# Kernel tuning notes

Measured on AMD Instinct MI355X. Metric: run time of the kernel, lower is better.

## Reference

```python
import jax, jax.numpy as jnp
import numpy as np

K = 10          # negatives per anchor (init k)
GAMMA = 1.0     # margin (init gamma)
CHUNK = 32      # anchor chunk for L1 cdist to bound [chunk, N, d] intermediate


def _l1_cdist(a, b):
    """Cityblock distances. a: [A, d], b: [N, d] -> [A, N], chunked over A."""
    A, d = a.shape
    a_c = a.reshape(A // CHUNK, CHUNK, d)
    def f(ac):  # ac: [CHUNK, d] -> [CHUNK, N]
        return jnp.sum(jnp.abs(ac[:, None, :] - b[None, :, :]), axis=-1)
    return jax.lax.map(f, a_c).reshape(A, b.shape[0])


def setup_inputs() -> dict:
    key = jax.random.key(0)
    k1, k2, k3, k4 = jax.random.split(key, 4)
    N, D, A = 20000, 128, 1024
    return {
        "out1": jax.random.normal(k1, (N, D), dtype=jnp.float32),
        "out2": jax.random.normal(k2, (N, D), dtype=jnp.float32),
        "anchor1": jax.random.randint(k3, (A,), 0, N),
        "anchor2": jax.random.randint(k4, (A,), 0, N),
    }


def reference(out1, out2, anchor1, anchor2):
    a1 = out1[anchor1]              # [A, D]
    a2 = out2[anchor2]              # [A, D]
    # neg sampling: k nearest (smallest L1 distance) rows of the other side
    d1 = _l1_cdist(a1, out2)        # [A, N]
    d2 = _l1_cdist(a2, out1)        # [A, N]
    neg1 = jnp.argsort(d1, axis=1)[:, :K]   # [A, K] indices into out2
    neg2 = jnp.argsort(d2, axis=1)[:, :K]   # [A, K] indices into out1
    neg_e1 = out2[neg1]             # [A, K, D]
    neg_e2 = out1[neg2]             # [A, K, D]
    A_pos = jnp.sum(jnp.abs(a1 - a2), axis=1)   # [A] positive L1 distance
    Dm = A_pos + GAMMA                           # [A]
    B1 = -jnp.sum(jnp.abs(a1[:, None, :] - neg_e1), axis=2)  # [A, K]
    L1 = jnp.sum(jax.nn.relu(Dm[:, None] + B1))
    B2 = -jnp.sum(jnp.abs(a2[:, None, :] - neg_e2), axis=2)  # [A, K]
    L2 = jnp.sum(jax.nn.relu(Dm[:, None] + B2))
    return (L1 + L2) / (anchor1.shape[0] * K)
```

## Files before the change

kernel.cpp:

```cpp
#include <hip/hip_runtime.h>

#define N_PTS 20000
#define DIMS  128
#define A_CNT 1024
#define KNEG  10
#define NTILES 157
#define NCHUNK (NTILES * 16)
#define NCHUNK_REAL 2500
#define BIGV  1e18f
#define BIGI  0x7F000000
#define CAND_CAP 768
#define PT_CAP   768
#define AB_BLOCKS 1024
#define QR_BLOCKS 625
#define RPART     1250

__device__ __forceinline__ unsigned int sad_u8(unsigned int a, unsigned int b, unsigned int c) {
#if __has_builtin(__builtin_amdgcn_sad_u8)
    return __builtin_amdgcn_sad_u8(a, b, c);
#else
    unsigned int d;
    asm("v_sad_u8 %0, %1, %2, %3" : "=v"(d) : "v"(a), "v"(b), "v"(c));
    return d;
#endif
}

__global__ void absmax_kernel(const float* __restrict__ a, const float* __restrict__ b,
                              float* __restrict__ wsAmax, float* __restrict__ outZero) {
    __shared__ float sm[4];
    const int n4 = N_PTS * DIMS / 4;
    const int stride = gridDim.x * blockDim.x;
    float m = 0.f;
    for (int i = blockIdx.x * blockDim.x + threadIdx.x; i < 2 * n4; i += stride) {
        const float4 v = (i < n4) ? ((const float4*)a)[i] : ((const float4*)b)[i - n4];
        m = fmaxf(m, fmaxf(fmaxf(fabsf(v.x), fabsf(v.y)), fmaxf(fabsf(v.z), fabsf(v.w))));
    }
#pragma unroll
    for (int s = 1; s < 64; s <<= 1) m = fmaxf(m, __shfl_xor(m, s, 64));
    if ((threadIdx.x & 63) == 0) sm[threadIdx.x >> 6] = m;
    __syncthreads();
    if (threadIdx.x == 0) {
        wsAmax[blockIdx.x] = fmaxf(fmaxf(sm[0], sm[1]), fmaxf(sm[2], sm[3]));
        if (blockIdx.x == 0) *outZero = 0.f;
    }
}

__global__ void quantR_kernel(const float* __restrict__ o1, const float* __restrict__ o2,
                              unsigned int* __restrict__ q1, unsigned int* __restrict__ q2,
                              float* __restrict__ Ra, float* __restrict__ Rb,
                              const float* __restrict__ wsAmax,
                              float* __restrict__ wsRmaxPart) {
    __shared__ float sm[4];
    __shared__ float sM;
    const int tid = threadIdx.x;
    {
        const float4 v = ((const float4*)wsAmax)[tid];
        float m = fmaxf(fmaxf(v.x, v.y), fmaxf(v.z, v.w));
#pragma unroll
        for (int s = 1; s < 64; s <<= 1) m = fmaxf(m, __shfl_xor(m, s, 64));
        if ((tid & 63) == 0) sm[tid >> 6] = m;
        __syncthreads();
        if (tid == 0) sM = fmaxf(fmaxf(sm[0], sm[1]), fmaxf(sm[2], sm[3]));
        __syncthreads();
    }
    const float M = sM;
    const float s = 127.0f / M;

    const int side = blockIdx.y;
    const float* src = side ? o2 : o1;
    unsigned int* dst = side ? q2 : q1;
    float* Rrow = side ? Rb : Ra;
    const int g = blockIdx.x * 256 + tid;
    const int row = g >> 3;
    const int sub = g & 7;
    const float4* s4 = (const float4*)(src + (size_t)row * DIMS + sub * 16);
    unsigned int* d = dst + (size_t)row * 32 + sub * 4;
    float rs = 0.f;
#pragma unroll
    for (int m = 0; m < 4; ++m) {
        const float4 v = s4[m];
        const float f0 = v.x * s + 127.0f, f1 = v.y * s + 127.0f;
        const float f2 = v.z * s + 127.0f, f3 = v.w * s + 127.0f;
        const float q0 = rintf(f0), q1v = rintf(f1), q2v = rintf(f2), q3 = rintf(f3);
        rs += fabsf(q0 - f0) + fabsf(q1v - f1) + fabsf(q2v - f2) + fabsf(q3 - f3);
        d[m] = (unsigned int)q0 | ((unsigned int)q1v << 8) |
               ((unsigned int)q2v << 16) | ((unsigned int)q3 << 24);
    }
    rs += __shfl_xor(rs, 1, 64);
    rs += __shfl_xor(rs, 2, 64);
    rs += __shfl_xor(rs, 4, 64);
    const float R = rs + 1.0f;
    if (sub == 0) Rrow[row] = R;
    float rm = R;
    rm = fmaxf(rm, __shfl_xor(rm, 8, 64));
    rm = fmaxf(rm, __shfl_xor(rm, 16, 64));
    rm = fmaxf(rm, __shfl_xor(rm, 32, 64));
    if ((tid & 63) == 0) sm[tid >> 6] = rm;
    __syncthreads();
    if (tid == 0)
        wsRmaxPart[blockIdx.y * QR_BLOCKS + blockIdx.x] =
            fmaxf(fmaxf(sm[0], sm[1]), fmaxf(sm[2], sm[3]));
}

__global__ __launch_bounds__(256, 4)
void dist_sad_kernel(const unsigned int* __restrict__ q1, const unsigned int* __restrict__ q2,
                     const int* __restrict__ anchor1, const int* __restrict__ anchor2,
                     unsigned short* __restrict__ minOut,
                     const float* __restrict__ wsRmaxPart, float* __restrict__ rmaxOut) {
    __shared__ unsigned int sP[128 * 32];

    const int tile = blockIdx.x;
    const int ag   = blockIdx.y;
    const int side = blockIdx.z;

    if (tile == 0 && ag == 0 && side == 0 && threadIdx.x < 64) {
        float r = 0.f;
        for (int i = threadIdx.x; i < RPART; i += 64) r = fmaxf(r, wsRmaxPart[i]);
#pragma unroll
        for (int s = 1; s < 64; s <<= 1) r = fmaxf(r, __shfl_xor(r, s, 64));
        if (threadIdx.x == 0) *rmaxOut = r;
    }

    const unsigned int* aData = side ? q2 : q1;
    const unsigned int* pData = side ? q1 : q2;
    const int*          aIdx  = side ? anchor2 : anchor1;

    const int tid = threadIdx.x;
    const int tx = tid & 15;
    const int ty = tid >> 4;

    const int4 aidx4 = ((const int4*)(aIdx + ag * 64))[ty];
    const unsigned int* aRow0 = aData + (size_t)aidx4.x * 32;
    const unsigned int* aRow1 = aData + (size_t)aidx4.y * 32;
    const unsigned int* aRow2 = aData + (size_t)aidx4.z * 32;
    const unsigned int* aRow3 = aData + (size_t)aidx4.w * 32;

    {
        const int rp = tid >> 1;
        const int h  = tid & 1;
        const int prow = tile * 128 + rp;
        const bool pvalid = prow < N_PTS;
        const uint4* pRow4 = (const uint4*)(pData + (size_t)prow * 32 + h * 16);
        const int rot = rp >> 3;
#pragma unroll
        for (int j = 0; j < 4; ++j) {
            const uint4 v = pvalid ? pRow4[j]
                                   : make_uint4(0xFFFFFFFFu, 0xFFFFFFFFu, 0xFFFFFFFFu, 0xFFFFFFFFu);
            const int blk = h * 4 + j;
            *(uint4*)&sP[rp * 32 + (((blk + rot) & 7) << 2)] = v;
        }
    }
    __syncthreads();

    unsigned int acc[4][8];
#pragma unroll
    for (int i = 0; i < 4; ++i)
#pragma unroll
        for (int j = 0; j < 8; ++j) acc[i][j] = 0u;

    const int tx8 = tx * 8;

#pragma unroll 2
    for (int bk = 0; bk < 8; ++bk) {
        uint4 A[4], P[8];
        A[0] = *(const uint4*)(aRow0 + bk * 4);
        A[1] = *(const uint4*)(aRow1 + bk * 4);
        A[2] = *(const uint4*)(aRow2 + bk * 4);
        A[3] = *(const uint4*)(aRow3 + bk * 4);
        const int pslot = ((bk + tx) & 7) << 2;
#pragma unroll
        for (int j = 0; j < 8; ++j) P[j] = *(const uint4*)&sP[(tx8 + j) * 32 + pslot];
#pragma unroll
        for (int i = 0; i < 4; ++i)
#pragma unroll
            for (int j = 0; j < 8; ++j) {
                unsigned int s = sad_u8(A[i].x, P[j].x, acc[i][j]);
                s = sad_u8(A[i].y, P[j].y, s);
                s = sad_u8(A[i].z, P[j].z, s);
                acc[i][j] = sad_u8(A[i].w, P[j].w, s);
            }
    }

    const int ty4 = ty * 4;
    const size_t outBase = (size_t)side * A_CNT * NCHUNK;
#pragma unroll
    for (int i = 0; i < 4; ++i) {
        unsigned int m = min(min(min(acc[i][0], acc[i][1]), min(acc[i][2], acc[i][3])),
                             min(min(acc[i][4], acc[i][5]), min(acc[i][6], acc[i][7])));
        minOut[outBase + (size_t)(ag * 64 + ty4 + i) * NCHUNK + tile * 16 + tx] =
            (unsigned short)m;
    }
}

__global__ __launch_bounds__(256, 4)
void select_kernel(const float* __restrict__ out1, const float* __restrict__ out2,
                   const unsigned int* __restrict__ q1, const unsigned int* __restrict__ q2,
                   const int* __restrict__ anchor1, const int* __restrict__ anchor2,
                   const unsigned short* __restrict__ minIn,
                   const float* __restrict__ R1, const float* __restrict__ R2,
                   const float* __restrict__ rmaxIn, float* __restrict__ out) {
    const int bid = blockIdx.x;
    const int side = bid >> 10;
    const int ai = bid & 1023;
    const int tid = threadIdx.x;
    const int lane = tid & 63;
    const int wv = tid >> 6;

    const float* aDataF = side ? out2 : out1;
    const float* pDataF = side ? out1 : out2;
    const unsigned int* aDataQ = side ? q2 : q1;
    const unsigned int* pDataQ = side ? q1 : q2;
    const float* Ranc = side ? R2 : R1;
    const int* aIdx = side ? anchor2 : anchor1;

    __shared__ int candCount, pointCount;
    __shared__ int candList[CAND_CAP];
    __shared__ int ptList[PT_CAP];
    __shared__ __align__(16) float sDist[PT_CAP];
    __shared__ int sMin[4];
    __shared__ int sCnt[4];
    __shared__ float wSum[4];
    __shared__ float sDm;

    const int arow = aIdx[ai];
    const uint4 qa4 = ((const uint4*)(aDataQ + (size_t)arow * 32))[lane & 7];
    if (tid == 0) { candCount = 0; pointCount = 0; }

    if (wv == 0) {
        const int r1 = anchor1[ai], r2 = anchor2[ai];
        const float2 x1 = ((const float2*)(out1 + (size_t)r1 * DIMS))[lane];
        const float2 x2 = ((const float2*)(out2 + (size_t)r2 * DIMS))[lane];
        float dm = fabsf(x1.x - x2.x) + fabsf(x1.y - x2.y);
#pragma unroll
        for (int s = 1; s < 64; s <<= 1) dm += __shfl_xor(dm, s, 64);
        if (lane == 0) sDm = dm + 1.0f;
    }

    const unsigned short* mbase = minIn + ((size_t)side * A_CNT + ai) * NCHUNK;
    int mv[10];
#pragma unroll
    for (int j = 0; j < 10; ++j) {
        const int c = tid + 256 * j;
        mv[j] = (c < NCHUNK_REAL) ? (int)mbase[c] : BIGI;
    }
    int lmin = BIGI;
#pragma unroll
    for (int j = 0; j < 10; ++j) lmin = min(lmin, mv[j]);
#pragma unroll
    for (int s = 1; s < 64; s <<= 1) lmin = min(lmin, __shfl_xor(lmin, s, 64));
    if (lane == 0) sMin[wv] = lmin;
    __syncthreads();
    const int m1 = min(min(sMin[0], sMin[1]), min(sMin[2], sMin[3]));

    int E = m1 + 192;
    for (;;) {
        int c = 0;
#pragma unroll
        for (int j = 0; j < 10; ++j) c += (mv[j] <= E) ? 1 : 0;
#pragma unroll
        for (int s = 1; s < 64; s <<= 1) c += __shfl_xor(c, s, 64);
        if (lane == 0) sCnt[wv] = c;
        __syncthreads();
        const int total = sCnt[0] + sCnt[1] + sCnt[2] + sCnt[3];
        __syncthreads();
        if (total >= KNEG) break;
        E += 192;
    }
    int lo = (E == m1 + 192) ? (m1 - 1) : (E - 192);
    int hi = E;
#pragma unroll
    for (int it = 0; it < 3; ++it) {
        const int mid = (lo + hi) >> 1;
        int c = 0;
#pragma unroll
        for (int j = 0; j < 10; ++j) c += (mv[j] <= mid) ? 1 : 0;
#pragma unroll
        for (int s = 1; s < 64; s <<= 1) c += __shfl_xor(c, s, 64);
        if (lane == 0) sCnt[wv] = c;
        __syncthreads();
        const int total = sCnt[0] + sCnt[1] + sCnt[2] + sCnt[3];
        __syncthreads();
        if (total >= KNEG) hi = mid; else lo = mid;
    }
    const float Rmax = *rmaxIn;
    const float thr = (float)hi + 2.0f * Ranc[arow] + 2.0f * Rmax + 4.0f;

#pragma unroll
    for (int j = 0; j < 10; ++j) {
        const int c = tid + 256 * j;
        if (c < NCHUNK_REAL && (float)mv[j] <= thr) {
            const int pos = atomicAdd(&candCount, 1);
            if (pos < CAND_CAP) candList[pos] = c;
        }
    }
    __syncthreads();
    const int cc = min(candCount, CAND_CAP);

    const int psub = lane >> 3;
    const int seg  = lane & 7;
    for (int s0 = wv * 4; s0 < cc; s0 += 16) {
        uint4 qp[4];
        int ptv[4];
#pragma unroll
        for (int u = 0; u < 4; ++u) {
            const int s = s0 + u;
            const int c = candList[(s < cc) ? s : s0];
            ptv[u] = c * 8 + psub;
            qp[u] = ((const uint4*)(pDataQ + (size_t)ptv[u] * 32))[seg];
        }
#pragma unroll
        for (int u = 0; u < 4; ++u) {
            unsigned int d = sad_u8(qa4.x, qp[u].x, 0u);
            d = sad_u8(qa4.y, qp[u].y, d);
            d = sad_u8(qa4.z, qp[u].z, d);
            d = sad_u8(qa4.w, qp[u].w, d);
            int di = (int)d;
            di += __shfl_xor(di, 1, 64);
            di += __shfl_xor(di, 2, 64);
            di += __shfl_xor(di, 4, 64);
            if ((s0 + u) < cc && seg == 0 && (float)di <= thr) {
                const int pos = atomicAdd(&pointCount, 1);
                if (pos < PT_CAP) ptList[pos] = ptv[u];
            }
        }
    }
    __syncthreads();
    const int pc = min(pointCount, PT_CAP);

    const int pt4 = tid >> 2;
    const int qq  = tid & 3;
    float4 av[8];
    {
        const float4* aF4 = (const float4*)(aDataF + (size_t)arow * DIMS) + qq * 8;
#pragma unroll
        for (int q = 0; q < 8; ++q) av[q] = aF4[q];
    }
    for (int base = 0; base < pc; base += 64) {
        const int idx = base + pt4;
        float s01 = 0.f, s23 = 0.f;
        if (idx < pc) {
            const int pt = ptList[idx];
            const float4* p4 = (const float4*)(pDataF + (size_t)pt * DIMS) + qq * 8;
#pragma unroll
            for (int q = 0; q < 8; ++q) {
                const float4 pv = p4[q];
                s01 += fabsf(av[q].x - pv.x) + fabsf(av[q].y - pv.y);
                s23 += fabsf(av[q].z - pv.z) + fabsf(av[q].w - pv.w);
            }
        }
        float s = s01 + s23;
        s += __shfl_xor(s, 1, 64);
        s += __shfl_xor(s, 2, 64);
        if (qq == 0 && idx < pc) sDist[idx] = s;
    }
    __syncthreads();

    const float dm = sDm;
    float contrib = 0.f;
    if (pc <= 256) {
        const int i0 = tid;
        const float v = (i0 < pc) ? sDist[i0] : BIGV;
        int r0 = 0;
        int j = 0;
        for (; j + 2 <= pc; j += 2) {
            const float2 vj = *(const float2*)&sDist[j];
            r0 += ((vj.x < v) || (vj.x == v && j < i0)) ? 1 : 0;
            r0 += ((vj.y < v) || (vj.y == v && (j + 1) < i0)) ? 1 : 0;
        }
        if (j < pc) {
            const float vj = sDist[j];
            r0 += ((vj < v) || (vj == v && j < i0)) ? 1 : 0;
        }
        if (i0 < pc && r0 < KNEG) contrib = fmaxf(dm - v, 0.f);
    } else {
        const int i0 = tid, i1 = tid + 256, i2 = tid + 512;
        float va = BIGV, vb = BIGV, vc = BIGV;
        if (i0 < pc) va = sDist[i0];
        if (i1 < pc) vb = sDist[i1];
        if (i2 < pc) vc = sDist[i2];
        int r0 = 0, r1 = 0, r2 = 0;
        for (int j = 0; j < pc; ++j) {
            const float vj = sDist[j];
            r0 += (vj < va) || (vj == va && j < i0);
            r1 += (vj < vb) || (vj == vb && j < i1);
            r2 += (vj < vc) || (vj == vc && j < i2);
        }
        if (i0 < pc && r0 < KNEG) contrib += fmaxf(dm - va, 0.f);
        if (i1 < pc && r1 < KNEG) contrib += fmaxf(dm - vb, 0.f);
        if (i2 < pc && r2 < KNEG) contrib += fmaxf(dm - vc, 0.f);
    }
#pragma unroll
    for (int s = 1; s < 64; s <<= 1) contrib += __shfl_xor(contrib, s, 64);
    if (lane == 0) wSum[wv] = contrib;
    __syncthreads();
    if (tid == 0)
        atomicAdd(out, (wSum[0] + wSum[1] + wSum[2] + wSum[3]) * (1.0f / (A_CNT * KNEG)));
}

extern "C" void kernel_launch(void* const* d_in, const int* in_sizes, int n_in,
                              void* d_out, int out_size, void* d_ws, size_t ws_size,
                              hipStream_t stream) {
    const float* out1    = (const float*)d_in[0];
    const float* out2    = (const float*)d_in[1];
    const int*   anchor1 = (const int*)d_in[2];
    const int*   anchor2 = (const int*)d_in[3];
    float* out = (float*)d_out;

    unsigned int* q1 = (unsigned int*)d_ws;
    unsigned int* q2 = q1 + (size_t)N_PTS * DIMS / 4;
    unsigned short* minbuf = (unsigned short*)(q2 + (size_t)N_PTS * DIMS / 4);
    float* R1 = (float*)(minbuf + (size_t)2 * A_CNT * NCHUNK);
    float* R2 = R1 + N_PTS;
    float* wsAmax = R2 + N_PTS;
    float* wsRmaxPart = wsAmax + AB_BLOCKS;
    float* rmax = wsRmaxPart + 1280;

    hipLaunchKernelGGL(absmax_kernel, dim3(AB_BLOCKS), dim3(256), 0, stream,
                       out1, out2, wsAmax, out);
    hipLaunchKernelGGL(quantR_kernel, dim3(QR_BLOCKS, 2), dim3(256), 0, stream,
                       out1, out2, q1, q2, R1, R2, wsAmax, wsRmaxPart);

    dim3 gridA(NTILES, 16, 2);
    hipLaunchKernelGGL(dist_sad_kernel, gridA, dim3(256), 0, stream,
                       q1, q2, anchor1, anchor2, minbuf, wsRmaxPart, rmax);
    hipLaunchKernelGGL(select_kernel, dim3(2048), dim3(256), 0, stream,
                       out1, out2, q1, q2, anchor1, anchor2, minbuf, R1, R2, rmax, out);
}
```

Measured before the change: 207.6 us.

## Store packed per-point SAD offsets to skip quantized recompute in select

The distance kernel now writes, next to each chunk minimum, a 32-bit word holding a 4-bit coarse offset per point (distance minus chunk min, shifted by 4 and clamped). The select kernel uses these packed offsets to filter individual points against the threshold directly. This drops the candidate-chunk list and the second quantized SAD pass over candidate points' rows. In exchange it adds a 2×1024×2512×4-byte write in the dist kernel and a read in select. The clamped and truncated offsets are a looser lower bound, so more points may pass the filter or overflow PT_CAP.

```diff
diff --git a/kernel.cpp b/kernel.cpp
--- a/kernel.cpp
+++ b/kernel.cpp
@@ -9,7 +9,6 @@
 #define NCHUNK_REAL 2500
 #define BIGV  1e18f
 #define BIGI  0x7F000000
-#define CAND_CAP 768
 #define PT_CAP   768
 #define AB_BLOCKS 1024
 #define QR_BLOCKS 625
@@ -105,7 +104,7 @@
 __global__ __launch_bounds__(256, 4)
 void dist_sad_kernel(const unsigned int* __restrict__ q1, const unsigned int* __restrict__ q2,
                      const int* __restrict__ anchor1, const int* __restrict__ anchor2,
-                     unsigned short* __restrict__ minOut,
+                     unsigned short* __restrict__ minOut, unsigned int* __restrict__ offOut,
                      const float* __restrict__ wsRmaxPart, float* __restrict__ rmaxOut) {
     __shared__ unsigned int sP[128 * 32];
 
@@ -185,18 +184,23 @@
     const size_t outBase = (size_t)side * A_CNT * NCHUNK;
 #pragma unroll
     for (int i = 0; i < 4; ++i) {
-        unsigned int m = min(min(min(acc[i][0], acc[i][1]), min(acc[i][2], acc[i][3])),
-                             min(min(acc[i][4], acc[i][5]), min(acc[i][6], acc[i][7])));
-        minOut[outBase + (size_t)(ag * 64 + ty4 + i) * NCHUNK + tile * 16 + tx] =
-            (unsigned short)m;
+        const unsigned int m = min(min(min(acc[i][0], acc[i][1]), min(acc[i][2], acc[i][3])),
+                                   min(min(acc[i][4], acc[i][5]), min(acc[i][6], acc[i][7])));
+        unsigned int pk = 0u;
+#pragma unroll
+        for (int j = 0; j < 8; ++j)
+            pk |= min(15u, (acc[i][j] - m) >> 4) << (4 * j);
+        const size_t cidx = outBase + (size_t)(ag * 64 + ty4 + i) * NCHUNK + tile * 16 + tx;
+        minOut[cidx] = (unsigned short)m;
+        offOut[cidx] = pk;
     }
 }
 
 __global__ __launch_bounds__(256, 4)
 void select_kernel(const float* __restrict__ out1, const float* __restrict__ out2,
-                   const unsigned int* __restrict__ q1, const unsigned int* __restrict__ q2,
                    const int* __restrict__ anchor1, const int* __restrict__ anchor2,
                    const unsigned short* __restrict__ minIn,
+                   const unsigned int* __restrict__ offIn,
                    const float* __restrict__ R1, const float* __restrict__ R2,
                    const float* __restrict__ rmaxIn, float* __restrict__ out) {
     const int bid = blockIdx.x;
@@ -208,13 +212,10 @@
 
     const float* aDataF = side ? out2 : out1;
     const float* pDataF = side ? out1 : out2;
-    const unsigned int* aDataQ = side ? q2 : q1;
-    const unsigned int* pDataQ = side ? q1 : q2;
     const float* Ranc = side ? R2 : R1;
     const int* aIdx = side ? anchor2 : anchor1;
 
-    __shared__ int candCount, pointCount;
-    __shared__ int candList[CAND_CAP];
+    __shared__ int pointCount;
     __shared__ int ptList[PT_CAP];
     __shared__ __align__(16) float sDist[PT_CAP];
     __shared__ int sMin[4];
@@ -223,8 +224,7 @@
     __shared__ float sDm;
 
     const int arow = aIdx[ai];
-    const uint4 qa4 = ((const uint4*)(aDataQ + (size_t)arow * 32))[lane & 7];
-    if (tid == 0) { candCount = 0; pointCount = 0; }
+    if (tid == 0) pointCount = 0;
 
     if (wv == 0) {
         const int r1 = anchor1[ai], r2 = anchor2[ai];
@@ -285,42 +285,20 @@
     const float Rmax = *rmaxIn;
     const float thr = (float)hi + 2.0f * Ranc[arow] + 2.0f * Rmax + 4.0f;
 
+    const unsigned int* offRow = offIn + ((size_t)side * A_CNT + ai) * NCHUNK;
 #pragma unroll
     for (int j = 0; j < 10; ++j) {
         const int c = tid + 256 * j;
         if (c < NCHUNK_REAL && (float)mv[j] <= thr) {
-            const int pos = atomicAdd(&candCount, 1);
-            if (pos < CAND_CAP) candList[pos] = c;
-        }
-    }
-    __syncthreads();
-    const int cc = min(candCount, CAND_CAP);
-
-    const int psub = lane >> 3;
-    const int seg  = lane & 7;
-    for (int s0 = wv * 4; s0 < cc; s0 += 16) {
-        uint4 qp[4];
-        int ptv[4];
-#pragma unroll
-        for (int u = 0; u < 4; ++u) {
-            const int s = s0 + u;
-            const int c = candList[(s < cc) ? s : s0];
-            ptv[u] = c * 8 + psub;
-            qp[u] = ((const uint4*)(pDataQ + (size_t)ptv[u] * 32))[seg];
-        }
-#pragma unroll
-        for (int u = 0; u < 4; ++u) {
-            unsigned int d = sad_u8(qa4.x, qp[u].x, 0u);
-            d = sad_u8(qa4.y, qp[u].y, d);
-            d = sad_u8(qa4.z, qp[u].z, d);
-            d = sad_u8(qa4.w, qp[u].w, d);
-            int di = (int)d;
-            di += __shfl_xor(di, 1, 64);
-            di += __shfl_xor(di, 2, 64);
-            di += __shfl_xor(di, 4, 64);
-            if ((s0 + u) < cc && seg == 0 && (float)di <= thr) {
-                const int pos = atomicAdd(&pointCount, 1);
-                if (pos < PT_CAP) ptList[pos] = ptv[u];
+            const unsigned int pk = offRow[c];
+            const int m = mv[j];
+#pragma unroll
+            for (int jj = 0; jj < 8; ++jj) {
+                const int bound = m + (int)(((pk >> (4 * jj)) & 15u) << 4);
+                if ((float)bound <= thr) {
+                    const int pos = atomicAdd(&pointCount, 1);
+                    if (pos < PT_CAP) ptList[pos] = c * 8 + jj;
+                }
             }
         }
     }
@@ -409,7 +387,8 @@
     unsigned int* q1 = (unsigned int*)d_ws;
     unsigned int* q2 = q1 + (size_t)N_PTS * DIMS / 4;
     unsigned short* minbuf = (unsigned short*)(q2 + (size_t)N_PTS * DIMS / 4);
-    float* R1 = (float*)(minbuf + (size_t)2 * A_CNT * NCHUNK);
+    unsigned int* offbuf = (unsigned int*)(minbuf + (size_t)2 * A_CNT * NCHUNK);
+    float* R1 = (float*)(offbuf + (size_t)2 * A_CNT * NCHUNK);
     float* R2 = R1 + N_PTS;
     float* wsAmax = R2 + N_PTS;
     float* wsRmaxPart = wsAmax + AB_BLOCKS;
@@ -422,7 +401,7 @@
 
     dim3 gridA(NTILES, 16, 2);
     hipLaunchKernelGGL(dist_sad_kernel, gridA, dim3(256), 0, stream,
-                       q1, q2, anchor1, anchor2, minbuf, wsRmaxPart, rmax);
+                       q1, q2, anchor1, anchor2, minbuf, offbuf, wsRmaxPart, rmax);
     hipLaunchKernelGGL(select_kernel, dim3(2048), dim3(256), 0, stream,
-                       out1, out2, q1, q2, anchor1, anchor2, minbuf, R1, R2, rmax, out);
-}
+                       out1, out2, anchor1, anchor2, minbuf, offbuf, R1, R2, rmax, out);
+}
```

Result: no change. 211.6 us (+1.9%).

## Fuse all four stages into one persistent cooperative kernel with grid syncs

Applied to the files above, without the earlier changes.

Replaces the four separate launches (absmax, quantise, SAD distance tiles, select) with a single persistent cooperative kernel that loops over virtual blocks and uses grid-wide syncs between stages. This is meant to remove launch overhead and the tail idle time between kernels. In exchange, the grid is capped at occupancy times CU count (at most 1024 blocks), and the grid barriers plus less flexible scheduling may reduce throughput in the heavy distance stage. If the cooperative launch is unavailable it falls back to the original launches.

```diff
diff --git a/kernel.cpp b/kernel.cpp
--- a/kernel.cpp
+++ b/kernel.cpp
@@ -1,4 +1,7 @@
 #include <hip/hip_runtime.h>
+#include <hip/hip_cooperative_groups.h>
+
+namespace cg = cooperative_groups;
 
 #define N_PTS 20000
 #define DIMS  128
@@ -77,14 +80,14 @@
     unsigned int* d = dst + (size_t)row * 32 + sub * 4;
     float rs = 0.f;
 #pragma unroll
-    for (int m = 0; m < 4; ++m) {
-        const float4 v = s4[m];
+    for (int m4 = 0; m4 < 4; ++m4) {
+        const float4 v = s4[m4];
         const float f0 = v.x * s + 127.0f, f1 = v.y * s + 127.0f;
         const float f2 = v.z * s + 127.0f, f3 = v.w * s + 127.0f;
         const float q0 = rintf(f0), q1v = rintf(f1), q2v = rintf(f2), q3 = rintf(f3);
         rs += fabsf(q0 - f0) + fabsf(q1v - f1) + fabsf(q2v - f2) + fabsf(q3 - f3);
-        d[m] = (unsigned int)q0 | ((unsigned int)q1v << 8) |
-               ((unsigned int)q2v << 16) | ((unsigned int)q3 << 24);
+        d[m4] = (unsigned int)q0 | ((unsigned int)q1v << 8) |
+                ((unsigned int)q2v << 16) | ((unsigned int)q3 << 24);
     }
     rs += __shfl_xor(rs, 1, 64);
     rs += __shfl_xor(rs, 2, 64);
@@ -108,7 +111,6 @@
                      unsigned short* __restrict__ minOut,
                      const float* __restrict__ wsRmaxPart, float* __restrict__ rmaxOut) {
     __shared__ unsigned int sP[128 * 32];
-
     const int tile = blockIdx.x;
     const int ag   = blockIdx.y;
     const int side = blockIdx.z;
@@ -124,7 +126,6 @@
     const unsigned int* aData = side ? q2 : q1;
     const unsigned int* pData = side ? q1 : q2;
     const int*          aIdx  = side ? anchor2 : anchor1;
-
     const int tid = threadIdx.x;
     const int tx = tid & 15;
     const int ty = tid >> 4;
@@ -157,7 +158,6 @@
     for (int i = 0; i < 4; ++i)
 #pragma unroll
         for (int j = 0; j < 8; ++j) acc[i][j] = 0u;
-
     const int tx8 = tx * 8;
 
 #pragma unroll 2
@@ -397,6 +397,381 @@
         atomicAdd(out, (wSum[0] + wSum[1] + wSum[2] + wSum[3]) * (1.0f / (A_CNT * KNEG)));
 }
 
+__global__ __launch_bounds__(256, 4)
+void fused_kernel(const float* __restrict__ out1, const float* __restrict__ out2,
+                  const int* __restrict__ anchor1, const int* __restrict__ anchor2,
+                  unsigned int* __restrict__ q1, unsigned int* __restrict__ q2,
+                  unsigned short* __restrict__ minbuf,
+                  float* __restrict__ R1, float* __restrict__ R2,
+                  float* __restrict__ wsAmax, float* __restrict__ wsRmaxPart,
+                  float* __restrict__ rmaxG, float* __restrict__ out) {
+    cg::grid_group grid = cg::this_grid();
+    const int bid = blockIdx.x;
+    const int nb  = gridDim.x;
+    const int tid = threadIdx.x;
+    const int lane = tid & 63;
+    const int wv = tid >> 6;
+
+    __shared__ unsigned int sP[128 * 32];
+    __shared__ float smax[4];
+    __shared__ float sM;
+
+    {
+        const int n4 = N_PTS * DIMS / 4;
+        float m = 0.f;
+        for (int i = bid * 256 + tid; i < 2 * n4; i += nb * 256) {
+            const float4 v = (i < n4) ? ((const float4*)out1)[i] : ((const float4*)out2)[i - n4];
+            m = fmaxf(m, fmaxf(fmaxf(fabsf(v.x), fabsf(v.y)), fmaxf(fabsf(v.z), fabsf(v.w))));
+        }
+#pragma unroll
+        for (int s = 1; s < 64; s <<= 1) m = fmaxf(m, __shfl_xor(m, s, 64));
+        if (lane == 0) smax[wv] = m;
+        __syncthreads();
+        if (tid == 0) {
+            wsAmax[bid] = fmaxf(fmaxf(smax[0], smax[1]), fmaxf(smax[2], smax[3]));
+            if (bid == 0) *out = 0.f;
+        }
+    }
+    grid.sync();
+
+    {
+        __syncthreads();
+        {
+            float m = 0.f;
+            for (int i = tid; i < nb; i += 256) m = fmaxf(m, wsAmax[i]);
+#pragma unroll
+            for (int s = 1; s < 64; s <<= 1) m = fmaxf(m, __shfl_xor(m, s, 64));
+            if (lane == 0) smax[wv] = m;
+            __syncthreads();
+            if (tid == 0) sM = fmaxf(fmaxf(smax[0], smax[1]), fmaxf(smax[2], smax[3]));
+            __syncthreads();
+        }
+        const float M = sM;
+        const float s = 127.0f / M;
+        for (int vb = bid; vb < 2 * QR_BLOCKS; vb += nb) {
+            __syncthreads();
+            const int side = (vb >= QR_BLOCKS) ? 1 : 0;
+            const int bx = side ? (vb - QR_BLOCKS) : vb;
+            const float* src = side ? out2 : out1;
+            unsigned int* dst = side ? q2 : q1;
+            float* Rrow = side ? R2 : R1;
+            const int g = bx * 256 + tid;
+            const int row = g >> 3;
+            const int sub = g & 7;
+            const float4* s4 = (const float4*)(src + (size_t)row * DIMS + sub * 16);
+            unsigned int* d = dst + (size_t)row * 32 + sub * 4;
+            float rs = 0.f;
+#pragma unroll
+            for (int m4 = 0; m4 < 4; ++m4) {
+                const float4 v = s4[m4];
+                const float f0 = v.x * s + 127.0f, f1 = v.y * s + 127.0f;
+                const float f2 = v.z * s + 127.0f, f3 = v.w * s + 127.0f;
+                const float q0 = rintf(f0), q1v = rintf(f1), q2v = rintf(f2), q3 = rintf(f3);
+                rs += fabsf(q0 - f0) + fabsf(q1v - f1) + fabsf(q2v - f2) + fabsf(q3 - f3);
+                d[m4] = (unsigned int)q0 | ((unsigned int)q1v << 8) |
+                        ((unsigned int)q2v << 16) | ((unsigned int)q3 << 24);
+            }
+            rs += __shfl_xor(rs, 1, 64);
+            rs += __shfl_xor(rs, 2, 64);
+            rs += __shfl_xor(rs, 4, 64);
+            const float R = rs + 1.0f;
+            if (sub == 0) Rrow[row] = R;
+            float rm = R;
+            rm = fmaxf(rm, __shfl_xor(rm, 8, 64));
+            rm = fmaxf(rm, __shfl_xor(rm, 16, 64));
+            rm = fmaxf(rm, __shfl_xor(rm, 32, 64));
+            if (lane == 0) smax[wv] = rm;
+            __syncthreads();
+            if (tid == 0)
+                wsRmaxPart[side * QR_BLOCKS + bx] =
+                    fmaxf(fmaxf(smax[0], smax[1]), fmaxf(smax[2], smax[3]));
+        }
+    }
+    grid.sync();
+
+    if (bid == 0 && tid < 64) {
+        float r = 0.f;
+        for (int i = tid; i < RPART; i += 64) r = fmaxf(r, wsRmaxPart[i]);
+#pragma unroll
+        for (int s = 1; s < 64; s <<= 1) r = fmaxf(r, __shfl_xor(r, s, 64));
+        if (tid == 0) *rmaxG = r;
+    }
+    {
+        const int tx = tid & 15;
+        const int ty = tid >> 4;
+        const int tx8 = tx * 8;
+        const int ty4 = ty * 4;
+        for (int vb = bid; vb < NTILES * 32; vb += nb) {
+            const int tile = vb % NTILES;
+            const int rest = vb / NTILES;
+            const int ag   = rest & 15;
+            const int side = rest >> 4;
+
+            const unsigned int* aData = side ? q2 : q1;
+            const unsigned int* pData = side ? q1 : q2;
+            const int*          aIdx  = side ? anchor2 : anchor1;
+
+            const int4 aidx4 = ((const int4*)(aIdx + ag * 64))[ty];
+            const unsigned int* aRow0 = aData + (size_t)aidx4.x * 32;
+            const unsigned int* aRow1 = aData + (size_t)aidx4.y * 32;
+            const unsigned int* aRow2 = aData + (size_t)aidx4.z * 32;
+            const unsigned int* aRow3 = aData + (size_t)aidx4.w * 32;
+
+            __syncthreads();
+            {
+                const int rp = tid >> 1;
+                const int h  = tid & 1;
+                const int prow = tile * 128 + rp;
+                const bool pvalid = prow < N_PTS;
+                const uint4* pRow4 = (const uint4*)(pData + (size_t)prow * 32 + h * 16);
+                const int rot = rp >> 3;
+#pragma unroll
+                for (int j = 0; j < 4; ++j) {
+                    const uint4 v = pvalid ? pRow4[j]
+                                           : make_uint4(0xFFFFFFFFu, 0xFFFFFFFFu,
+                                                        0xFFFFFFFFu, 0xFFFFFFFFu);
+                    const int blk = h * 4 + j;
+                    *(uint4*)&sP[rp * 32 + (((blk + rot) & 7) << 2)] = v;
+                }
+            }
+            __syncthreads();
+
+            unsigned int acc[4][8];
+#pragma unroll
+            for (int i = 0; i < 4; ++i)
+#pragma unroll
+                for (int j = 0; j < 8; ++j) acc[i][j] = 0u;
+
+#pragma unroll 2
+            for (int bk = 0; bk < 8; ++bk) {
+                uint4 A[4], P[8];
+                A[0] = *(const uint4*)(aRow0 + bk * 4);
+                A[1] = *(const uint4*)(aRow1 + bk * 4);
+                A[2] = *(const uint4*)(aRow2 + bk * 4);
+                A[3] = *(const uint4*)(aRow3 + bk * 4);
+                const int pslot = ((bk + tx) & 7) << 2;
+#pragma unroll
+                for (int j = 0; j < 8; ++j) P[j] = *(const uint4*)&sP[(tx8 + j) * 32 + pslot];
+#pragma unroll
+                for (int i = 0; i < 4; ++i)
+#pragma unroll
+                    for (int j = 0; j < 8; ++j) {
+                        unsigned int sacc = sad_u8(A[i].x, P[j].x, acc[i][j]);
+                        sacc = sad_u8(A[i].y, P[j].y, sacc);
+                        sacc = sad_u8(A[i].z, P[j].z, sacc);
+                        acc[i][j] = sad_u8(A[i].w, P[j].w, sacc);
+                    }
+            }
+
+            const size_t outBase = (size_t)side * A_CNT * NCHUNK;
+#pragma unroll
+            for (int i = 0; i < 4; ++i) {
+                unsigned int m = min(min(min(acc[i][0], acc[i][1]), min(acc[i][2], acc[i][3])),
+                                     min(min(acc[i][4], acc[i][5]), min(acc[i][6], acc[i][7])));
+                minbuf[outBase + (size_t)(ag * 64 + ty4 + i) * NCHUNK + tile * 16 + tx] =
+                    (unsigned short)m;
+            }
+        }
+    }
+    grid.sync();
+
+    {
+        int* candList = (int*)sP;
+        int* ptList   = candList + CAND_CAP;
+        float* sDist  = (float*)(ptList + PT_CAP);
+        int* misc     = (int*)(sDist + PT_CAP);
+        float* wSum = (float*)(misc + 10);
+        const float Rmax = *rmaxG;
+
+        for (int vt = bid; vt < 2 * A_CNT; vt += nb) {
+            __syncthreads();
+            const int side = vt >> 10;
+            const int ai = vt & 1023;
+
+            const float* aDataF = side ? out2 : out1;
+            const float* pDataF = side ? out1 : out2;
+            const unsigned int* aDataQ = side ? q2 : q1;
+            const unsigned int* pDataQ = side ? q1 : q2;
+            const float* Ranc = side ? R2 : R1;
+            const int* aIdx = side ? anchor2 : anchor1;
+
+            const int arow = aIdx[ai];
+            const uint4 qa4 = ((const uint4*)(aDataQ + (size_t)arow * 32))[lane & 7];
+            if (tid == 0) { misc[0] = 0; misc[1] = 0; }
+
+            if (wv == 0) {
+                const int r1 = anchor1[ai], r2 = anchor2[ai];
+                const float2 x1 = ((const float2*)(out1 + (size_t)r1 * DIMS))[lane];
+                const float2 x2 = ((const float2*)(out2 + (size_t)r2 * DIMS))[lane];
+                float dm = fabsf(x1.x - x2.x) + fabsf(x1.y - x2.y);
+#pragma unroll
+                for (int s = 1; s < 64; s <<= 1) dm += __shfl_xor(dm, s, 64);
+                if (lane == 0) ((float*)misc)[14] = dm + 1.0f;
+            }
+
+            const unsigned short* mbase = minbuf + ((size_t)side * A_CNT + ai) * NCHUNK;
+            int mv[10];
+#pragma unroll
+            for (int j = 0; j < 10; ++j) {
+                const int c = tid + 256 * j;
+                mv[j] = (c < NCHUNK_REAL) ? (int)mbase[c] : BIGI;
+            }
+            int lmin = BIGI;
+#pragma unroll
+            for (int j = 0; j < 10; ++j) lmin = min(lmin, mv[j]);
+#pragma unroll
+            for (int s = 1; s < 64; s <<= 1) lmin = min(lmin, __shfl_xor(lmin, s, 64));
+            if (lane == 0) misc[2 + wv] = lmin;
+            __syncthreads();
+            const int m1 = min(min(misc[2], misc[3]), min(misc[4], misc[5]));
+
+            int E = m1 + 192;
+            for (;;) {
+                int c = 0;
+#pragma unroll
+                for (int j = 0; j < 10; ++j) c += (mv[j] <= E) ? 1 : 0;
+#pragma unroll
+                for (int s = 1; s < 64; s <<= 1) c += __shfl_xor(c, s, 64);
+                if (lane == 0) misc[6 + wv] = c;
+                __syncthreads();
+                const int total = misc[6] + misc[7] + misc[8] + misc[9];
+                __syncthreads();
+                if (total >= KNEG) break;
+                E += 192;
+            }
+            int lo = (E == m1 + 192) ? (m1 - 1) : (E - 192);
+            int hi = E;
+#pragma unroll
+            for (int it = 0; it < 3; ++it) {
+                const int mid = (lo + hi) >> 1;
+                int c = 0;
+#pragma unroll
+                for (int j = 0; j < 10; ++j) c += (mv[j] <= mid) ? 1 : 0;
+#pragma unroll
+                for (int s = 1; s < 64; s <<= 1) c += __shfl_xor(c, s, 64);
+                if (lane == 0) misc[6 + wv] = c;
+                __syncthreads();
+                const int total = misc[6] + misc[7] + misc[8] + misc[9];
+                __syncthreads();
+                if (total >= KNEG) hi = mid; else lo = mid;
+            }
+            const float thr = (float)hi + 2.0f * Ranc[arow] + 2.0f * Rmax + 4.0f;
+
+#pragma unroll
+            for (int j = 0; j < 10; ++j) {
+                const int c = tid + 256 * j;
+                if (c < NCHUNK_REAL && (float)mv[j] <= thr) {
+                    const int pos = atomicAdd(&misc[0], 1);
+                    if (pos < CAND_CAP) candList[pos] = c;
+                }
+            }
+            __syncthreads();
+            const int cc = min(misc[0], CAND_CAP);
+
+            const int psub = lane >> 3;
+            const int seg  = lane & 7;
+            for (int s0 = wv * 4; s0 < cc; s0 += 16) {
+                uint4 qp[4];
+                int ptv[4];
+#pragma unroll
+                for (int u = 0; u < 4; ++u) {
+                    const int s = s0 + u;
+                    const int c = candList[(s < cc) ? s : s0];
+                    ptv[u] = c * 8 + psub;
+                    qp[u] = ((const uint4*)(pDataQ + (size_t)ptv[u] * 32))[seg];
+                }
+#pragma unroll
+                for (int u = 0; u < 4; ++u) {
+                    unsigned int d = sad_u8(qa4.x, qp[u].x, 0u);
+                    d = sad_u8(qa4.y, qp[u].y, d);
+                    d = sad_u8(qa4.z, qp[u].z, d);
+                    d = sad_u8(qa4.w, qp[u].w, d);
+                    int di = (int)d;
+                    di += __shfl_xor(di, 1, 64);
+                    di += __shfl_xor(di, 2, 64);
+                    di += __shfl_xor(di, 4, 64);
+                    if ((s0 + u) < cc && seg == 0 && (float)di <= thr) {
+                        const int pos = atomicAdd(&misc[1], 1);
+                        if (pos < PT_CAP) ptList[pos] = ptv[u];
+                    }
+                }
+            }
+            __syncthreads();
+            const int pc = min(misc[1], PT_CAP);
+
+            const int pt4 = tid >> 2;
+            const int qq  = tid & 3;
+            float4 av[8];
+            {
+                const float4* aF4 = (const float4*)(aDataF + (size_t)arow * DIMS) + qq * 8;
+#pragma unroll
+                for (int q = 0; q < 8; ++q) av[q] = aF4[q];
+            }
+            for (int base = 0; base < pc; base += 64) {
+                const int idx = base + pt4;
+                float s01 = 0.f, s23 = 0.f;
+                if (idx < pc) {
+                    const int pt = ptList[idx];
+                    const float4* p4 = (const float4*)(pDataF + (size_t)pt * DIMS) + qq * 8;
+#pragma unroll
+                    for (int q = 0; q < 8; ++q) {
+                        const float4 pv = p4[q];
+                        s01 += fabsf(av[q].x - pv.x) + fabsf(av[q].y - pv.y);
+                        s23 += fabsf(av[q].z - pv.z) + fabsf(av[q].w - pv.w);
+                    }
+                }
+                float sacc = s01 + s23;
+                sacc += __shfl_xor(sacc, 1, 64);
+                sacc += __shfl_xor(sacc, 2, 64);
+                if (qq == 0 && idx < pc) sDist[idx] = sacc;
+            }
+            __syncthreads();
+
+            const float dm = ((float*)misc)[14];
+            float contrib = 0.f;
+            if (pc <= 256) {
+                const int i0 = tid;
+                const float v = (i0 < pc) ? sDist[i0] : BIGV;
+                int r0 = 0;
+                int j = 0;
+                for (; j + 2 <= pc; j += 2) {
+                    const float2 vj = *(const float2*)&sDist[j];
+                    r0 += ((vj.x < v) || (vj.x == v && j < i0)) ? 1 : 0;
+                    r0 += ((vj.y < v) || (vj.y == v && (j + 1) < i0)) ? 1 : 0;
+                }
+                if (j < pc) {
+                    const float vj = sDist[j];
+                    r0 += ((vj < v) || (vj == v && j < i0)) ? 1 : 0;
+                }
+                if (i0 < pc && r0 < KNEG) contrib = fmaxf(dm - v, 0.f);
+            } else {
+                const int i0 = tid, i1 = tid + 256, i2 = tid + 512;
+                float va = BIGV, vb2 = BIGV, vc = BIGV;
+                if (i0 < pc) va = sDist[i0];
+                if (i1 < pc) vb2 = sDist[i1];
+                if (i2 < pc) vc = sDist[i2];
+                int r0 = 0, r1 = 0, r2 = 0;
+                for (int j = 0; j < pc; ++j) {
+                    const float vj = sDist[j];
+                    r0 += (vj < va) || (vj == va && j < i0);
+                    r1 += (vj < vb2) || (vj == vb2 && j < i1);
+                    r2 += (vj < vc) || (vj == vc && j < i2);
+                }
+                if (i0 < pc && r0 < KNEG) contrib += fmaxf(dm - va, 0.f);
+                if (i1 < pc && r1 < KNEG) contrib += fmaxf(dm - vb2, 0.f);
+                if (i2 < pc && r2 < KNEG) contrib += fmaxf(dm - vc, 0.f);
+            }
+#pragma unroll
+            for (int s = 1; s < 64; s <<= 1) contrib += __shfl_xor(contrib, s, 64);
+            if (lane == 0) wSum[wv] = contrib;
+            __syncthreads();
+            if (tid == 0)
+                atomicAdd(out, (wSum[0] + wSum[1] + wSum[2] + wSum[3]) *
+                               (1.0f / (A_CNT * KNEG)));
+        }
+    }
+}
+
 extern "C" void kernel_launch(void* const* d_in, const int* in_sizes, int n_in,
                               void* d_out, int out_size, void* d_ws, size_t ws_size,
                               hipStream_t stream) {
@@ -415,11 +790,46 @@
     float* wsRmaxPart = wsAmax + AB_BLOCKS;
     float* rmax = wsRmaxPart + 1280;
 
+    static int coopMode = -1;
+    static int coopGrid = 0;
+    if (coopMode == -1) {
+        int dev = 0;
+        (void)hipGetDevice(&dev);
+        int coopOK = 0;
+        (void)hipDeviceGetAttribute(&coopOK, hipDeviceAttributeCooperativeLaunch, dev);
+        int cus = 0;
+        (void)hipDeviceGetAttribute(&cus, hipDeviceAttributeMultiprocessorCount, dev);
+        int nb = 0;
+        hipError_t oe = hipOccupancyMaxActiveBlocksPerMultiprocessor(
+            &nb, (const void*)fused_kernel, 256, 0);
+        if (coopOK && oe == hipSuccess && nb > 0 && cus > 0) {
+            long g = (long)nb * (long)cus;
+            if (g > 1024) g = 1024;
+            coopGrid = (int)g;
+            coopMode = (coopGrid >= 256) ? 1 : 0;
+        } else {
+            coopMode = 0;
+        }
+    }
+
+    if (coopMode == 1) {
+        void* args[] = {
+            (void*)&out1, (void*)&out2, (void*)&anchor1, (void*)&anchor2,
+            (void*)&q1, (void*)&q2, (void*)&minbuf,
+            (void*)&R1, (void*)&R2, (void*)&wsAmax, (void*)&wsRmaxPart,
+            (void*)&rmax, (void*)&out
+        };
+        hipError_t err = hipLaunchCooperativeKernel((const void*)fused_kernel,
+                                                    dim3(coopGrid), dim3(256),
+                                                    args, 0, stream);
+        if (err == hipSuccess) return;
+        coopMode = 0;
+    }
+
     hipLaunchKernelGGL(absmax_kernel, dim3(AB_BLOCKS), dim3(256), 0, stream,
                        out1, out2, wsAmax, out);
     hipLaunchKernelGGL(quantR_kernel, dim3(QR_BLOCKS, 2), dim3(256), 0, stream,
                        out1, out2, q1, q2, R1, R2, wsAmax, wsRmaxPart);
-
     dim3 gridA(NTILES, 16, 2);
     hipLaunchKernelGGL(dist_sad_kernel, gridA, dim3(256), 0, stream,
                        q1, q2, anchor1, anchor2, minbuf, wsRmaxPart, rmax);
```

After: 427.0 us. 2.06x slower.
